# Kernel tuning notes

Measured on AMD Instinct MI355X. Metric: run time of the kernel, lower is better.

## Reference

```python
import jax, jax.numpy as jnp
import numpy as np

N = 100000      # nodes
DEG = 16        # avg degree
E = N * DEG     # edges
D = 128         # feature dim
U = 128         # output units


def setup_inputs() -> dict:
    key = jax.random.key(0)
    k1, k2, k3, k4 = jax.random.split(key, 4)
    node_features = jax.random.normal(k1, (N, D), dtype=jnp.float32)
    # every row has exactly DEG entries so the 'mean' combiner never divides by zero
    edge_rows = jnp.arange(E, dtype=jnp.int64) // DEG
    edge_cols = jax.random.randint(k2, (E,), 0, N, dtype=jnp.int64)
    edge_weights = jax.random.uniform(k3, (E,), dtype=jnp.float32, minval=0.1, maxval=1.0)
    W = jax.random.normal(k4, (D, U), dtype=jnp.float32) * (1.0 / np.sqrt(D))
    b = jnp.zeros((U,), dtype=jnp.float32)
    return {"node_features": node_features, "edge_rows": edge_rows,
            "edge_cols": edge_cols, "edge_weights": edge_weights, "W": W, "b": b}


def reference(node_features, edge_rows, edge_cols, edge_weights, W, b):
    # embedding_lookup_sparse_v2 with combiner='mean':
    # agg[i] = sum_j w_ij * feat[j] / sum_j w_ij
    gathered = node_features[edge_cols] * edge_weights[:, None]   # [E, D]
    num = jax.ops.segment_sum(gathered, edge_rows, num_segments=N)  # [N, D]
    den = jax.ops.segment_sum(edge_weights, edge_rows, num_segments=N)  # [N]
    agg = num / den[:, None]
    # Dense(units, activation='relu'); dropout/l2_norm are built but not applied in call()
    return jax.nn.relu(agg @ W + b)
```

## Files before the change

kernel.cpp:

```cpp
#include <hip/hip_runtime.h>

#define N_NODES 100000
#define DEG 16
#define D_DIM 128
#define U_DIM 128
#define M_TILE 128

typedef __bf16 bf16x8 __attribute__((ext_vector_type(8)));
typedef float f32x4 __attribute__((ext_vector_type(4)));

__device__ __forceinline__ unsigned short f2bf(float x) {
    unsigned int u = __float_as_uint(x);
    u += 0x7fffu + ((u >> 16) & 1u);
    return (unsigned short)(u >> 16);
}

__global__ void cast_w_kernel(const float* __restrict__ W,
                              unsigned short* __restrict__ WT) {
    int t = blockIdx.x * 256 + threadIdx.x;
    int k = t >> 7, n = t & 127;
    WT[n * 128 + k] = f2bf(W[t]);
}

__global__ __launch_bounds__(256)
void ymat_kernel(const float* __restrict__ feat,
                 const unsigned short* __restrict__ WT,
                 unsigned short* __restrict__ Y) {
    const int lane = threadIdx.x & 63;
    const int wv = threadIdx.x >> 6;
    const int block0 = blockIdx.x * M_TILE;
    const int quad = lane >> 4;
    const int l15 = lane & 15;

    f32x4 acc[2][8];
    #pragma unroll
    for (int mi = 0; mi < 2; ++mi)
        #pragma unroll
        for (int ni = 0; ni < 8; ++ni)
            acc[mi][ni] = (f32x4){0.f, 0.f, 0.f, 0.f};

    #pragma unroll
    for (int kc = 0; kc < 4; ++kc) {
        bf16x8 bfr[8];
        #pragma unroll
        for (int ni = 0; ni < 8; ++ni)
            bfr[ni] = *(const bf16x8*)(WT + (ni * 16 + l15) * 128 + kc * 32 + quad * 8);
        bf16x8 afr[2];
        #pragma unroll
        for (int mi = 0; mi < 2; ++mi) {
            int row = block0 + wv * 32 + mi * 16 + l15;
            if (row >= N_NODES) row = N_NODES - 1;
            const float* ap = feat + (size_t)row * D_DIM + kc * 32 + quad * 8;
            const float4 a0 = *(const float4*)ap;
            const float4 a1 = *(const float4*)(ap + 4);
            union { unsigned short us[8]; bf16x8 b; } pk;
            pk.us[0] = f2bf(a0.x); pk.us[1] = f2bf(a0.y);
            pk.us[2] = f2bf(a0.z); pk.us[3] = f2bf(a0.w);
            pk.us[4] = f2bf(a1.x); pk.us[5] = f2bf(a1.y);
            pk.us[6] = f2bf(a1.z); pk.us[7] = f2bf(a1.w);
            afr[mi] = pk.b;
        }
        #pragma unroll
        for (int mi = 0; mi < 2; ++mi)
            #pragma unroll
            for (int ni = 0; ni < 8; ++ni)
                acc[mi][ni] = __builtin_amdgcn_mfma_f32_16x16x32_bf16(afr[mi], bfr[ni], acc[mi][ni], 0, 0, 0);
    }

    #pragma unroll
    for (int mi = 0; mi < 2; ++mi)
        #pragma unroll
        for (int r = 0; r < 4; ++r) {
            const int row = block0 + wv * 32 + mi * 16 + quad * 4 + r;
            if (row < N_NODES) {
                #pragma unroll
                for (int ni = 0; ni < 8; ++ni)
                    Y[(size_t)row * U_DIM + ni * 16 + l15] = f2bf(acc[mi][ni][r]);
            }
        }
}

__global__ __launch_bounds__(256, 6)
void agg_kernel(const unsigned int* __restrict__ Ybf2,
                const int* __restrict__ cols,
                const float* __restrict__ wts,
                const float* __restrict__ bias,
                float* __restrict__ out) {
    const int node = blockIdx.x * 4 + (threadIdx.x >> 6);
    const int lane = threadIdx.x & 63;
    const int e0 = node * DEG;

    int cc[DEG];
    float ww[DEG];
    #pragma unroll
    for (int q = 0; q < 4; ++q) {
        const int4 c4 = *(const int4*)(cols + e0 + q * 4);
        const float4 w4 = *(const float4*)(wts + e0 + q * 4);
        cc[q * 4 + 0] = c4.x; cc[q * 4 + 1] = c4.y; cc[q * 4 + 2] = c4.z; cc[q * 4 + 3] = c4.w;
        ww[q * 4 + 0] = w4.x; ww[q * 4 + 1] = w4.y; ww[q * 4 + 2] = w4.z; ww[q * 4 + 3] = w4.w;
    }

    unsigned int p[DEG];
    #pragma unroll
    for (int e = 0; e < DEG; ++e)
        p[e] = Ybf2[(size_t)cc[e] * 64 + lane];

    float ax = 0.f, ay = 0.f, den = 0.f;
    #pragma unroll
    for (int e = 0; e < DEG; ++e) {
        const float fx = __uint_as_float(p[e] << 16);
        const float fy = __uint_as_float(p[e] & 0xffff0000u);
        ax = fmaf(ww[e], fx, ax);
        ay = fmaf(ww[e], fy, ay);
        den += ww[e];
    }
    const float inv = 1.0f / den;
    const float2 bv = ((const float2*)bias)[lane];
    float2 o;
    o.x = fmaxf(fmaf(ax, inv, bv.x), 0.f);
    o.y = fmaxf(fmaf(ay, inv, bv.y), 0.f);
    ((float2*)(out + (size_t)node * U_DIM))[lane] = o;
}

extern "C" void kernel_launch(void* const* d_in, const int* in_sizes, int n_in,
                              void* d_out, int out_size, void* d_ws, size_t ws_size,
                              hipStream_t stream) {
    const float* feat = (const float*)d_in[0];
    const int* cols  = (const int*)d_in[2];
    const float* wts = (const float*)d_in[3];
    const float* W   = (const float*)d_in[4];
    const float* b   = (const float*)d_in[5];
    float* out = (float*)d_out;

    unsigned short* wt_bf = (unsigned short*)d_ws;
    unsigned short* Y     = (unsigned short*)((char*)d_ws + 32768);

    cast_w_kernel<<<16384 / 256, 256, 0, stream>>>(W, wt_bf);

    const int nblocks = (N_NODES + M_TILE - 1) / M_TILE;
    ymat_kernel<<<nblocks, 256, 0, stream>>>(feat, wt_bf, Y);

    agg_kernel<<<N_NODES / 4, 256, 0, stream>>>(
        (const unsigned int*)Y, cols, wts, b, out);
}
```

Baseline: 185.2 us.

## Slice Y into column-sliced layout so gather working set fits cache per slice

Y is stored as 8 column slices of 16 bf16 values each (N x 16 per slice), and the aggregation grid is split by slice. Each slice is 3.2MB, so random neighbour gathers within a slice can hit L2/LLC instead of touching the full 25.6MB table. The catch is that each thread now gathers 32-byte rows with 8 threads per node, and edge indices and weights are re-read once per slice (8x index traffic). Block-to-slice interleaving (slice = blockIdx & 7) also means concurrent blocks span all slices, which may weaken the locality benefit.

```diff
diff --git a/kernel.cpp b/kernel.cpp
--- a/kernel.cpp
+++ b/kernel.cpp
@@ -2,9 +2,12 @@
 
 #define N_NODES 100000
 #define DEG 16
+#define E_EDGES (N_NODES * DEG)
 #define D_DIM 128
 #define U_DIM 128
 #define M_TILE 128
+#define N_SLICES 8
+#define NODES_PER_BLOCK 128
 
 typedef __bf16 bf16x8 __attribute__((ext_vector_type(8)));
 typedef float f32x4 __attribute__((ext_vector_type(4)));
@@ -25,7 +28,7 @@
 __global__ __launch_bounds__(256)
 void ymat_kernel(const float* __restrict__ feat,
                  const unsigned short* __restrict__ WT,
-                 unsigned short* __restrict__ Y) {
+                 unsigned short* __restrict__ Ys) {
     const int lane = threadIdx.x & 63;
     const int wv = threadIdx.x >> 6;
     const int block0 = blockIdx.x * M_TILE;
@@ -75,51 +78,66 @@
             if (row < N_NODES) {
                 #pragma unroll
                 for (int ni = 0; ni < 8; ++ni)
-                    Y[(size_t)row * U_DIM + ni * 16 + l15] = f2bf(acc[mi][ni][r]);
+                    Ys[(size_t)ni * (N_NODES * 16) + (size_t)row * 16 + l15] =
+                        f2bf(acc[mi][ni][r]);
             }
         }
 }
 
 __global__ __launch_bounds__(256, 6)
-void agg_kernel(const unsigned int* __restrict__ Ybf2,
+void agg_kernel(const unsigned int* __restrict__ Ys_u32,
                 const int* __restrict__ cols,
                 const float* __restrict__ wts,
                 const float* __restrict__ bias,
                 float* __restrict__ out) {
-    const int node = blockIdx.x * 4 + (threadIdx.x >> 6);
-    const int lane = threadIdx.x & 63;
-    const int e0 = node * DEG;
+    const int slice = blockIdx.x & (N_SLICES - 1);
+    const int nb = blockIdx.x >> 3;
+    const int n0 = nb * NODES_PER_BLOCK;
+    const int j = threadIdx.x & 7;
+    const int nl = threadIdx.x >> 3;
 
-    int cc[DEG];
-    float ww[DEG];
+    const float2 bv = ((const float2*)bias)[slice * 8 + j];
+    const unsigned int* Sbase = Ys_u32 + (size_t)slice * N_NODES * 8;
+
     #pragma unroll
-    for (int q = 0; q < 4; ++q) {
-        const int4 c4 = *(const int4*)(cols + e0 + q * 4);
-        const float4 w4 = *(const float4*)(wts + e0 + q * 4);
-        cc[q * 4 + 0] = c4.x; cc[q * 4 + 1] = c4.y; cc[q * 4 + 2] = c4.z; cc[q * 4 + 3] = c4.w;
-        ww[q * 4 + 0] = w4.x; ww[q * 4 + 1] = w4.y; ww[q * 4 + 2] = w4.z; ww[q * 4 + 3] = w4.w;
+    for (int it = 0; it < 4; ++it) {
+        const int node = n0 + it * 32 + nl;
+        if (node >= N_NODES) continue;
+
+        const int4* cp = (const int4*)(cols + node * DEG);
+        const float4* wp = (const float4*)(wts + node * DEG);
+        int cc[DEG];
+        float ww[DEG];
+        #pragma unroll
+        for (int q = 0; q < 4; ++q) {
+            const int4 c4 = cp[q];
+            const float4 w4 = wp[q];
+            cc[q * 4 + 0] = c4.x; cc[q * 4 + 1] = c4.y;
+            cc[q * 4 + 2] = c4.z; cc[q * 4 + 3] = c4.w;
+            ww[q * 4 + 0] = w4.x; ww[q * 4 + 1] = w4.y;
+            ww[q * 4 + 2] = w4.z; ww[q * 4 + 3] = w4.w;
+        }
+
+        unsigned int p[DEG];
+        #pragma unroll
+        for (int e = 0; e < DEG; ++e)
+            p[e] = Sbase[(size_t)cc[e] * 8 + j];
+
+        float ax = 0.f, ay = 0.f, den = 0.f;
+        #pragma unroll
+        for (int e = 0; e < DEG; ++e) {
+            const float fx = __uint_as_float(p[e] << 16);
+            const float fy = __uint_as_float(p[e] & 0xffff0000u);
+            ax = fmaf(ww[e], fx, ax);
+            ay = fmaf(ww[e], fy, ay);
+            den += ww[e];
+        }
+        const float inv = 1.0f / den;
+        float2 o;
+        o.x = fmaxf(fmaf(ax, inv, bv.x), 0.f);
+        o.y = fmaxf(fmaf(ay, inv, bv.y), 0.f);
+        ((float2*)(out + (size_t)node * U_DIM + slice * 16))[j] = o;
     }
-
-    unsigned int p[DEG];
-    #pragma unroll
-    for (int e = 0; e < DEG; ++e)
-        p[e] = Ybf2[(size_t)cc[e] * 64 + lane];
-
-    float ax = 0.f, ay = 0.f, den = 0.f;
-    #pragma unroll
-    for (int e = 0; e < DEG; ++e) {
-        const float fx = __uint_as_float(p[e] << 16);
-        const float fy = __uint_as_float(p[e] & 0xffff0000u);
-        ax = fmaf(ww[e], fx, ax);
-        ay = fmaf(ww[e], fy, ay);
-        den += ww[e];
-    }
-    const float inv = 1.0f / den;
-    const float2 bv = ((const float2*)bias)[lane];
-    float2 o;
-    o.x = fmaxf(fmaf(ax, inv, bv.x), 0.f);
-    o.y = fmaxf(fmaf(ay, inv, bv.y), 0.f);
-    ((float2*)(out + (size_t)node * U_DIM))[lane] = o;
 }
 
 extern "C" void kernel_launch(void* const* d_in, const int* in_sizes, int n_in,
@@ -133,13 +151,13 @@
     float* out = (float*)d_out;
 
     unsigned short* wt_bf = (unsigned short*)d_ws;
-    unsigned short* Y     = (unsigned short*)((char*)d_ws + 32768);
+    unsigned short* Ys    = (unsigned short*)((char*)d_ws + 32768);
 
     cast_w_kernel<<<16384 / 256, 256, 0, stream>>>(W, wt_bf);
 
     const int nblocks = (N_NODES + M_TILE - 1) / M_TILE;
-    ymat_kernel<<<nblocks, 256, 0, stream>>>(feat, wt_bf, Y);
+    ymat_kernel<<<nblocks, 256, 0, stream>>>(feat, wt_bf, Ys);
 
-    agg_kernel<<<N_NODES / 4, 256, 0, stream>>>(
-        (const unsigned int*)Y, cols, wts, b, out);
+    agg_kernel<<<N_SLICES * nblocks, 256, 0, stream>>>(
+        (const unsigned int*)Ys, cols, wts, b, out);
 }
```

Result: slower. 219.7 us (+18.7%).

## Drop W cast kernel, fold bias into Y, use 16-byte gathers in aggregation

Applied to the files above, without the earlier changes.

Removes the separate weight-cast kernel by having each GEMM wave load and convert its own slice of W straight into registers. It also swaps the MFMA operand roles so each wave covers 32 output units across 128 nodes. Bias is added when Y is computed, which is valid only because the mean weights sum to one and relu comes after the mean. The aggregation kernel now gives each node 16 threads, each gathering 16 bytes per neighbor row, with non-temporal output stores, to get wider memory transactions and fewer instructions per gathered byte. The trade-offs are one bf16 rounding of the biased value and lower occupancy from the launch bound of 4.

```diff
diff --git a/kernel.cpp b/kernel.cpp
--- a/kernel.cpp
+++ b/kernel.cpp
@@ -4,7 +4,6 @@
 #define DEG 16
 #define D_DIM 128
 #define U_DIM 128
-#define M_TILE 128
 
 typedef __bf16 bf16x8 __attribute__((ext_vector_type(8)));
 typedef float f32x4 __attribute__((ext_vector_type(4)));
@@ -14,112 +13,128 @@
     u += 0x7fffu + ((u >> 16) & 1u);
     return (unsigned short)(u >> 16);
 }
-
-__global__ void cast_w_kernel(const float* __restrict__ W,
-                              unsigned short* __restrict__ WT) {
-    int t = blockIdx.x * 256 + threadIdx.x;
-    int k = t >> 7, n = t & 127;
-    WT[n * 128 + k] = f2bf(W[t]);
+__device__ __forceinline__ unsigned int pack2(float a, float b) {
+    return (unsigned int)f2bf(a) | ((unsigned int)f2bf(b) << 16);
 }
 
 __global__ __launch_bounds__(256)
 void ymat_kernel(const float* __restrict__ feat,
-                 const unsigned short* __restrict__ WT,
+                 const float* __restrict__ W,
+                 const float* __restrict__ bias,
                  unsigned short* __restrict__ Y) {
     const int lane = threadIdx.x & 63;
     const int wv = threadIdx.x >> 6;
-    const int block0 = blockIdx.x * M_TILE;
     const int quad = lane >> 4;
     const int l15 = lane & 15;
+    const int n0 = blockIdx.x * 128;
+    const int u_base = wv * 32;
 
-    f32x4 acc[2][8];
+    bf16x8 afr[2][4];
     #pragma unroll
-    for (int mi = 0; mi < 2; ++mi)
+    for (int ni = 0; ni < 2; ++ni) {
+        const int u = u_base + ni * 16 + l15;
         #pragma unroll
-        for (int ni = 0; ni < 8; ++ni)
-            acc[mi][ni] = (f32x4){0.f, 0.f, 0.f, 0.f};
+        for (int kc = 0; kc < 4; ++kc) {
+            union { unsigned short us[8]; bf16x8 v; } pk;
+            #pragma unroll
+            for (int j = 0; j < 8; ++j)
+                pk.us[j] = f2bf(W[(kc * 32 + quad * 8 + j) * 128 + u]);
+            afr[ni][kc] = pk.v;
+        }
+    }
+    float4 bv0 = *(const float4*)(bias + u_base + quad * 4);
+    float4 bv1 = *(const float4*)(bias + u_base + 16 + quad * 4);
 
-    #pragma unroll
-    for (int kc = 0; kc < 4; ++kc) {
-        bf16x8 bfr[8];
+    for (int mi = 0; mi < 8; ++mi) {
+        const int node = n0 + mi * 16 + l15;
+        const int rowc = node < N_NODES ? node : N_NODES - 1;
+        bf16x8 bfr[4];
         #pragma unroll
-        for (int ni = 0; ni < 8; ++ni)
-            bfr[ni] = *(const bf16x8*)(WT + (ni * 16 + l15) * 128 + kc * 32 + quad * 8);
-        bf16x8 afr[2];
-        #pragma unroll
-        for (int mi = 0; mi < 2; ++mi) {
-            int row = block0 + wv * 32 + mi * 16 + l15;
-            if (row >= N_NODES) row = N_NODES - 1;
-            const float* ap = feat + (size_t)row * D_DIM + kc * 32 + quad * 8;
+        for (int kc = 0; kc < 4; ++kc) {
+            const float* ap = feat + (size_t)rowc * D_DIM + kc * 32 + quad * 8;
             const float4 a0 = *(const float4*)ap;
             const float4 a1 = *(const float4*)(ap + 4);
-            union { unsigned short us[8]; bf16x8 b; } pk;
+            union { unsigned short us[8]; bf16x8 v; } pk;
             pk.us[0] = f2bf(a0.x); pk.us[1] = f2bf(a0.y);
             pk.us[2] = f2bf(a0.z); pk.us[3] = f2bf(a0.w);
             pk.us[4] = f2bf(a1.x); pk.us[5] = f2bf(a1.y);
             pk.us[6] = f2bf(a1.z); pk.us[7] = f2bf(a1.w);
-            afr[mi] = pk.b;
+            bfr[kc] = pk.v;
         }
+        f32x4 acc0 = (f32x4){0.f, 0.f, 0.f, 0.f};
+        f32x4 acc1 = (f32x4){0.f, 0.f, 0.f, 0.f};
         #pragma unroll
-        for (int mi = 0; mi < 2; ++mi)
-            #pragma unroll
-            for (int ni = 0; ni < 8; ++ni)
-                acc[mi][ni] = __builtin_amdgcn_mfma_f32_16x16x32_bf16(afr[mi], bfr[ni], acc[mi][ni], 0, 0, 0);
+        for (int kc = 0; kc < 4; ++kc) {
+            acc0 = __builtin_amdgcn_mfma_f32_16x16x32_bf16(afr[0][kc], bfr[kc], acc0, 0, 0, 0);
+            acc1 = __builtin_amdgcn_mfma_f32_16x16x32_bf16(afr[1][kc], bfr[kc], acc1, 0, 0, 0);
+        }
+        if (node < N_NODES) {
+            unsigned int* yp = (unsigned int*)(Y + (size_t)node * U_DIM + u_base + quad * 4);
+            uint2 s0, s1;
+            s0.x = pack2(acc0[0] + bv0.x, acc0[1] + bv0.y);
+            s0.y = pack2(acc0[2] + bv0.z, acc0[3] + bv0.w);
+            s1.x = pack2(acc1[0] + bv1.x, acc1[1] + bv1.y);
+            s1.y = pack2(acc1[2] + bv1.z, acc1[3] + bv1.w);
+            *(uint2*)yp = s0;
+            *(uint2*)(yp + 8) = s1;
+        }
     }
-
-    #pragma unroll
-    for (int mi = 0; mi < 2; ++mi)
-        #pragma unroll
-        for (int r = 0; r < 4; ++r) {
-            const int row = block0 + wv * 32 + mi * 16 + quad * 4 + r;
-            if (row < N_NODES) {
-                #pragma unroll
-                for (int ni = 0; ni < 8; ++ni)
-                    Y[(size_t)row * U_DIM + ni * 16 + l15] = f2bf(acc[mi][ni][r]);
-            }
-        }
 }
 
-__global__ __launch_bounds__(256, 6)
-void agg_kernel(const unsigned int* __restrict__ Ybf2,
+__global__ __launch_bounds__(256, 4)
+void agg_kernel(const unsigned short* __restrict__ Y,
                 const int* __restrict__ cols,
                 const float* __restrict__ wts,
-                const float* __restrict__ bias,
                 float* __restrict__ out) {
-    const int node = blockIdx.x * 4 + (threadIdx.x >> 6);
-    const int lane = threadIdx.x & 63;
+    const int node = blockIdx.x * 16 + (threadIdx.x >> 4);
+    const int d = threadIdx.x & 15;
     const int e0 = node * DEG;
 
     int cc[DEG];
     float ww[DEG];
     #pragma unroll
     for (int q = 0; q < 4; ++q) {
-        const int4 c4 = *(const int4*)(cols + e0 + q * 4);
-        const float4 w4 = *(const float4*)(wts + e0 + q * 4);
-        cc[q * 4 + 0] = c4.x; cc[q * 4 + 1] = c4.y; cc[q * 4 + 2] = c4.z; cc[q * 4 + 3] = c4.w;
-        ww[q * 4 + 0] = w4.x; ww[q * 4 + 1] = w4.y; ww[q * 4 + 2] = w4.z; ww[q * 4 + 3] = w4.w;
+        const int4 c4 = *(const int4*)(cols + e0 + 4 * q);
+        const float4 w4 = *(const float4*)(wts + e0 + 4 * q);
+        cc[4 * q + 0] = c4.x; cc[4 * q + 1] = c4.y;
+        cc[4 * q + 2] = c4.z; cc[4 * q + 3] = c4.w;
+        ww[4 * q + 0] = w4.x; ww[4 * q + 1] = w4.y;
+        ww[4 * q + 2] = w4.z; ww[4 * q + 3] = w4.w;
     }
+    float den = 0.f;
+    #pragma unroll
+    for (int e = 0; e < DEG; ++e) den += ww[e];
 
-    unsigned int p[DEG];
+    float a0 = 0.f, a1 = 0.f, a2 = 0.f, a3 = 0.f;
+    float a4 = 0.f, a5 = 0.f, a6 = 0.f, a7 = 0.f;
     #pragma unroll
-    for (int e = 0; e < DEG; ++e)
-        p[e] = Ybf2[(size_t)cc[e] * 64 + lane];
-
-    float ax = 0.f, ay = 0.f, den = 0.f;
-    #pragma unroll
-    for (int e = 0; e < DEG; ++e) {
-        const float fx = __uint_as_float(p[e] << 16);
-        const float fy = __uint_as_float(p[e] & 0xffff0000u);
-        ax = fmaf(ww[e], fx, ax);
-        ay = fmaf(ww[e], fy, ay);
-        den += ww[e];
+    for (int h = 0; h < 2; ++h) {
+        uint4 p[8];
+        #pragma unroll
+        for (int e = 0; e < 8; ++e)
+            p[e] = *(const uint4*)(Y + (size_t)cc[h * 8 + e] * U_DIM + d * 8);
+        #pragma unroll
+        for (int e = 0; e < 8; ++e) {
+            const float w = ww[h * 8 + e];
+            a0 = fmaf(w, __uint_as_float(p[e].x << 16), a0);
+            a1 = fmaf(w, __uint_as_float(p[e].x & 0xffff0000u), a1);
+            a2 = fmaf(w, __uint_as_float(p[e].y << 16), a2);
+            a3 = fmaf(w, __uint_as_float(p[e].y & 0xffff0000u), a3);
+            a4 = fmaf(w, __uint_as_float(p[e].z << 16), a4);
+            a5 = fmaf(w, __uint_as_float(p[e].z & 0xffff0000u), a5);
+            a6 = fmaf(w, __uint_as_float(p[e].w << 16), a6);
+            a7 = fmaf(w, __uint_as_float(p[e].w & 0xffff0000u), a7);
+        }
     }
     const float inv = 1.0f / den;
-    const float2 bv = ((const float2*)bias)[lane];
-    float2 o;
-    o.x = fmaxf(fmaf(ax, inv, bv.x), 0.f);
-    o.y = fmaxf(fmaf(ay, inv, bv.y), 0.f);
-    ((float2*)(out + (size_t)node * U_DIM))[lane] = o;
+    f32x4 o0, o1;
+    o0[0] = fmaxf(a0 * inv, 0.f); o0[1] = fmaxf(a1 * inv, 0.f);
+    o0[2] = fmaxf(a2 * inv, 0.f); o0[3] = fmaxf(a3 * inv, 0.f);
+    o1[0] = fmaxf(a4 * inv, 0.f); o1[1] = fmaxf(a5 * inv, 0.f);
+    o1[2] = fmaxf(a6 * inv, 0.f); o1[3] = fmaxf(a7 * inv, 0.f);
+    f32x4* op = (f32x4*)(out + (size_t)node * U_DIM + d * 8);
+    __builtin_nontemporal_store(o0, op);
+    __builtin_nontemporal_store(o1, op + 1);
 }
 
 extern "C" void kernel_launch(void* const* d_in, const int* in_sizes, int n_in,
@@ -132,14 +147,10 @@
     const float* b   = (const float*)d_in[5];
     float* out = (float*)d_out;
 
-    unsigned short* wt_bf = (unsigned short*)d_ws;
-    unsigned short* Y     = (unsigned short*)((char*)d_ws + 32768);
+    unsigned short* Y = (unsigned short*)d_ws;
 
-    cast_w_kernel<<<16384 / 256, 256, 0, stream>>>(W, wt_bf);
+    const int nblocks = (N_NODES + 127) / 128;
+    ymat_kernel<<<nblocks, 256, 0, stream>>>(feat, W, b, Y);
 
-    const int nblocks = (N_NODES + M_TILE - 1) / M_TILE;
-    ymat_kernel<<<nblocks, 256, 0, stream>>>(feat, wt_bf, Y);
-
-    agg_kernel<<<N_NODES / 4, 256, 0, stream>>>(
-        (const unsigned int*)Y, cols, wts, b, out);
+    agg_kernel<<<N_NODES / 16, 256, 0, stream>>>(Y, cols, wts, out);
 }
```

Result: slower. 196.0 us (+5.9%).
